# Kernel optimization log

Hardware: AMD Instinct MI355X
Metric: run time of the kernel (lower is better)

## Reference

```python
import jax, jax.numpy as jnp
import numpy as np

DIM = 2048
NH = 16
Q_LORA = 1536
KV_LORA = 512
NOPE = 128
ROPE = 64
VDIM = 128
QK = NOPE + ROPE  # 192
B, S = 2, 2048
EPS = 1.1920929e-07  # torch.finfo(float32).eps (nn.RMSNorm default)


def linear(x, w, b):
    return jnp.einsum('...i,oi->...o', x, w) + b


def rmsnorm(x, w):
    ms = jnp.mean(x * x, axis=-1, keepdims=True)
    return x * jax.lax.rsqrt(ms + EPS) * w


def rope(x, cos, sin):
    # x: [B,S,H,d] interleaved pairs; cos/sin: [S, d//2]
    x = x.reshape(*x.shape[:-1], -1, 2)
    x0, x1 = x[..., 0], x[..., 1]
    c = cos[None, :, None, :]
    s = sin[None, :, None, :]
    y0 = x0 * c - x1 * s
    y1 = x0 * s + x1 * c
    return jnp.stack([y0, y1], axis=-1).reshape(*x.shape[:-2], -1)


def setup_inputs() -> dict:
    key = jax.random.key(0)
    ks = jax.random.split(key, 12)
    sd = 0.02
    x = jax.random.normal(ks[0], (B, S, DIM), dtype=jnp.float32)
    freqs = jax.random.normal(ks[1], (S, ROPE // 2), dtype=jnp.float32)
    causal_mask = jnp.where(jnp.triu(jnp.ones((S, S), bool), k=1), -1e9, 0.0).astype(jnp.float32)
    inp = dict(x=x, freqs=freqs, causal_mask=causal_mask)
    inp['Wq_down_w'] = sd * jax.random.normal(ks[2], (Q_LORA, DIM), dtype=jnp.float32)
    inp['Wq_down_b'] = jnp.zeros((Q_LORA,), jnp.float32)
    inp['q_norm_w'] = jnp.ones((Q_LORA,), jnp.float32)
    inp['Wq_up_w'] = sd * jax.random.normal(ks[3], (NH * QK, Q_LORA), dtype=jnp.float32)
    inp['Wq_up_b'] = jnp.zeros((NH * QK,), jnp.float32)
    inp['Wkv_down_w'] = sd * jax.random.normal(ks[4], (KV_LORA + ROPE, DIM), dtype=jnp.float32)
    inp['Wkv_down_b'] = jnp.zeros((KV_LORA + ROPE,), jnp.float32)
    inp['kv_norm_w'] = jnp.ones((KV_LORA,), jnp.float32)
    inp['Wkv_up_w'] = sd * jax.random.normal(ks[5], (NH * (NOPE + VDIM), KV_LORA), dtype=jnp.float32)
    inp['Wkv_up_b'] = jnp.zeros((NH * (NOPE + VDIM),), jnp.float32)
    inp['Wo_w'] = sd * jax.random.normal(ks[6], (DIM, NH * VDIM), dtype=jnp.float32)
    inp['Wo_b'] = jnp.zeros((DIM,), jnp.float32)
    return inp


def reference(x, freqs, causal_mask, Wq_down_w, Wq_down_b, q_norm_w, Wq_up_w, Wq_up_b,
              Wkv_down_w, Wkv_down_b, kv_norm_w, Wkv_up_w, Wkv_up_b, Wo_w, Wo_b):
    cos, sin = jnp.cos(freqs), jnp.sin(freqs)
    scale = QK ** -0.5
    # Q path: low-rank down, RMSNorm, up
    q_lat = rmsnorm(linear(x, Wq_down_w, Wq_down_b), q_norm_w)
    Q = linear(q_lat, Wq_up_w, Wq_up_b).reshape(B, S, NH, QK)
    Q_nope, Q_rope = Q[..., :NOPE], Q[..., NOPE:]
    Q_rope = rope(Q_rope, cos, sin)
    Q = jnp.concatenate([Q_nope, Q_rope], axis=-1)  # [B,S,H,QK]
    # KV path: shared latent + decoupled rope key
    kv_kr = linear(x, Wkv_down_w, Wkv_down_b)
    kv_lat, K_rope = kv_kr[..., :KV_LORA], kv_kr[..., KV_LORA:]
    kv_lat = rmsnorm(kv_lat, kv_norm_w)
    K_rope = rope(K_rope[:, :, None, :], cos, sin)  # [B,S,1,ROPE]
    kv = linear(kv_lat, Wkv_up_w, Wkv_up_b).reshape(B, S, NH, NOPE + VDIM)
    K_nope, V = kv[..., :NOPE], kv[..., NOPE:]
    K = jnp.concatenate([K_nope, jnp.broadcast_to(K_rope, (B, S, NH, ROPE))], axis=-1)
    # attention
    scores = jnp.einsum('bqhd,bkhd->bhqk', Q, K) * scale + causal_mask[None, None]
    attn = jax.nn.softmax(scores, axis=-1)
    out = jnp.einsum('bhqk,bkhd->bqhd', attn, V).reshape(B, S, NH * VDIM)
    return linear(out, Wo_w, Wo_b)
```

## Files before the change

kernel.cpp:

```cpp
#include <hip/hip_runtime.h>
#include <hip/hip_bf16.h>

#define DIMD 2048
#define NHD 16
#define QLORA 1536
#define KVLORA 512
#define QKD 192
#define BBD 2
#define SSD 2048
#define BSD (BBD*SSD)
#define KVPAD 640
#define BHN (BBD*NHD)
#define EPSF 1.1920929e-07f
#define SCALEF 0.07216878364870322f

typedef __hip_bfloat16 bf16;
typedef __attribute__((ext_vector_type(8))) short short8;
typedef __attribute__((ext_vector_type(4))) float floatx4;

typedef __attribute__((address_space(1))) char as1_char;
typedef __attribute__((address_space(3))) char as3_char;
#define GLD16(g, l) __builtin_amdgcn_global_load_lds((as1_char*)(g), (as3_char*)(l), 16, 0, 0)

__device__ __forceinline__ float block_sum(float x) {
#pragma unroll
  for (int o = 32; o > 0; o >>= 1) x += __shfl_xor(x, o, 64);
  __shared__ float red[4];
  __syncthreads();
  if ((threadIdx.x & 63) == 0) red[threadIdx.x >> 6] = x;
  __syncthreads();
  return red[0] + red[1] + red[2] + red[3];
}

template<bool STORE_BF16>
__global__ __launch_bounds__(256)
void gemm_bt(const bf16* __restrict__ A, const bf16* __restrict__ Bm,
             const float* __restrict__ bias, void* __restrict__ Cp,
             int M, int N, int K, long sA, long sB, long sC, int ldc)
{
  int m0 = blockIdx.y * 128, n0 = blockIdx.x * 128;
  long z = blockIdx.z;
  A  += z * sA;
  Bm += z * sB;

  __shared__ __align__(16) bf16 Asm[128 * 32];
  __shared__ __align__(16) bf16 Bsm[128 * 32];

  const int tid  = threadIdx.x;
  const int lane = tid & 63;
  const int wv   = tid >> 6;
  const int wm   = (wv >> 1) << 6;
  const int wn   = (wv & 1) << 6;
  const int fr   = lane & 15;
  const int q8   = (lane >> 4) << 3;

  floatx4 acc[4][4];
#pragma unroll
  for (int i = 0; i < 4; ++i)
#pragma unroll
    for (int j = 0; j < 4; ++j)
      acc[i][j] = (floatx4){0.f, 0.f, 0.f, 0.f};

  for (int k0 = 0; k0 < K; k0 += 32) {
    __syncthreads();
#pragma unroll
    for (int it = 0; it < 2; ++it) {
      int seg = it * 256 + tid;
      int row = seg >> 2, cs = seg & 3;
      GLD16(A  + (long)(m0 + row) * K + k0 + cs * 8, &Asm[(it * 256 + wv * 64) * 8]);
      GLD16(Bm + (long)(n0 + row) * K + k0 + cs * 8, &Bsm[(it * 256 + wv * 64) * 8]);
    }
    __syncthreads();

    short8 fa[4], fb[4];
#pragma unroll
    for (int t = 0; t < 4; ++t) fa[t] = *(const short8*)&Asm[(wm + t * 16 + fr) * 32 + q8];
#pragma unroll
    for (int t = 0; t < 4; ++t) fb[t] = *(const short8*)&Bsm[(wn + t * 16 + fr) * 32 + q8];
#pragma unroll
    for (int i = 0; i < 4; ++i)
#pragma unroll
      for (int j = 0; j < 4; ++j)
        acc[i][j] = __builtin_amdgcn_mfma_f32_16x16x32_bf16(fa[i], fb[j], acc[i][j], 0, 0, 0);
  }

  long cb = z * sC;
  int rq = (lane >> 4) * 4;
#pragma unroll
  for (int i = 0; i < 4; ++i) {
#pragma unroll
    for (int j = 0; j < 4; ++j) {
      int col = n0 + wn + j * 16 + fr;
      float bv = bias ? bias[col] : 0.f;
#pragma unroll
      for (int r = 0; r < 4; ++r) {
        int rowg = m0 + wm + i * 16 + rq + r;
        float v = acc[i][j][r] + bv;
        if (STORE_BF16)
          ((bf16*)Cp)[cb + (long)rowg * ldc + col] = __float2bfloat16(v);
        else
          ((float*)Cp)[cb + (long)rowg * ldc + col] = v;
      }
    }
  }
}

__global__ __launch_bounds__(512, 2)
void flash_attn(const bf16* __restrict__ Qh, const bf16* __restrict__ Kh,
                const bf16* __restrict__ Vt, bf16* __restrict__ attnall)
{
  const int p = blockIdx.x;
  const int z = blockIdx.y;
  const int b = z >> 4, h = z & 15;

  const bf16* Qg = Qh + (long)z * SSD * QKD;
  const bf16* Kg = Kh + (long)z * SSD * QKD;
  const bf16* Vg = Vt + (long)z * 128 * SSD;

  __shared__ __align__(16) bf16 Ksm[6 * 4096];
  __shared__ __align__(16) bf16 Vsm[4 * 4096];
  bf16* Psm = Ksm;

  const int tid  = threadIdx.x;
  const int lane = tid & 63;
  const int wv   = tid >> 6;
  const int fr   = lane & 15;
  const int g4   = lane >> 4;
  const int q8   = g4 << 3;
  const int srow = tid >> 2;
  const int scs  = tid & 3;

#pragma unroll 1
  for (int t = 0; t < 2; ++t) {
    const int qt = t ? p : 15 - p;
    const int q0 = qt * 128;

    __syncthreads();
#pragma unroll
    for (int c = 0; c < 6; ++c)
      GLD16(Qg + (long)(q0 + srow) * QKD + c * 32 + scs * 8, &Ksm[c * 4096 + wv * 512]);
    __syncthreads();
    short8 qf[6];
#pragma unroll
    for (int c = 0; c < 6; ++c)
      qf[c] = *(const short8*)&Ksm[c * 4096 + (wv * 16 + fr) * 32 + q8];

    floatx4 oacc[8];
#pragma unroll
    for (int n = 0; n < 8; ++n) oacc[n] = (floatx4){0.f, 0.f, 0.f, 0.f};
    float mi[4], li[4];
#pragma unroll
    for (int r = 0; r < 4; ++r) { mi[r] = -1e30f; li[r] = 0.f; }

    for (int j = 0; j <= qt; ++j) {
      const int jb = j * 128;
      __syncthreads();
#pragma unroll
      for (int c = 0; c < 6; ++c)
        GLD16(Kg + (long)(jb + srow) * QKD + c * 32 + scs * 8, &Ksm[c * 4096 + wv * 512]);
#pragma unroll
      for (int c = 0; c < 4; ++c)
        GLD16(Vg + (long)srow * SSD + jb + c * 32 + scs * 8, &Vsm[c * 4096 + wv * 512]);
      __syncthreads();

      floatx4 sacc[8];
#pragma unroll
      for (int n = 0; n < 8; ++n) sacc[n] = (floatx4){0.f, 0.f, 0.f, 0.f};
#pragma unroll
      for (int c = 0; c < 6; ++c) {
#pragma unroll
        for (int n = 0; n < 8; ++n) {
          short8 fb = *(const short8*)&Ksm[c * 4096 + (n * 16 + fr) * 32 + q8];
          sacc[n] = __builtin_amdgcn_mfma_f32_16x16x32_bf16(qf[c], fb, sacc[n], 0, 0, 0);
        }
      }

      const bool diag = (j == qt);
#pragma unroll
      for (int r = 0; r < 4; ++r) {
        int rowg = q0 + wv * 16 + g4 * 4 + r;
        float mx = -1e30f;
#pragma unroll
        for (int n = 0; n < 8; ++n) {
          float v = sacc[n][r] * SCALEF;
          if (diag && (jb + n * 16 + fr) > rowg) v = -1e30f;
          sacc[n][r] = v;
          mx = fmaxf(mx, v);
        }
#pragma unroll
        for (int off = 1; off < 16; off <<= 1) mx = fmaxf(mx, __shfl_xor(mx, off, 64));
        float mnew = fmaxf(mi[r], mx);
        float alpha = __expf(mi[r] - mnew);
        mi[r] = mnew;
        float rs = 0.f;
#pragma unroll
        for (int n = 0; n < 8; ++n) {
          float pv = __expf(sacc[n][r] - mnew);
          sacc[n][r] = pv;
          rs += pv;
        }
#pragma unroll
        for (int off = 1; off < 16; off <<= 1) rs += __shfl_xor(rs, off, 64);
        li[r] = li[r] * alpha + rs;
#pragma unroll
        for (int n = 0; n < 8; ++n) oacc[n][r] *= alpha;
      }

      __syncthreads();
#pragma unroll
      for (int n = 0; n < 8; ++n) {
        int c2 = n >> 1;
        int col = (n & 1) * 16 + fr;
#pragma unroll
        for (int r = 0; r < 4; ++r) {
          int m = wv * 16 + g4 * 4 + r;
          Psm[c2 * 4096 + m * 32 + col] = __float2bfloat16(sacc[n][r]);
        }
      }

#pragma unroll
      for (int c2 = 0; c2 < 4; ++c2) {
        short8 pf = *(const short8*)&Psm[c2 * 4096 + (wv * 16 + fr) * 32 + q8];
#pragma unroll
        for (int dn = 0; dn < 8; ++dn) {
          short8 vf = *(const short8*)&Vsm[c2 * 4096 + (dn * 16 + fr) * 32 + q8];
          oacc[dn] = __builtin_amdgcn_mfma_f32_16x16x32_bf16(pf, vf, oacc[dn], 0, 0, 0);
        }
      }
    }

#pragma unroll
    for (int r = 0; r < 4; ++r) {
      float inv = 1.f / li[r];
      int m = q0 + wv * 16 + g4 * 4 + r;
      bf16* orow = attnall + ((long)(b * SSD + m) * NHD + h) * 128;
#pragma unroll
      for (int dn = 0; dn < 8; ++dn)
        orow[dn * 16 + fr] = __float2bfloat16(oacc[dn][r] * inv);
    }
  }
}

__device__ __forceinline__ void cvt4(const float* __restrict__ s, bf16* __restrict__ d,
                                     long se, long de) {
  float4 v = *(const float4*)(s + se);
  union { bf16 h[4]; uint2 u; } o;
  o.h[0] = __float2bfloat16(v.x); o.h[1] = __float2bfloat16(v.y);
  o.h[2] = __float2bfloat16(v.z); o.h[3] = __float2bfloat16(v.w);
  *(uint2*)(d + de) = o.u;
}

#define NX4   ((long)BSD * DIMD / 4)
#define NQD4  ((long)QLORA * DIMD / 4)
#define NQU4  ((long)3072 * QLORA / 4)
#define NKVD4 ((long)KVPAD * DIMD / 4)
#define NKVU4 ((long)4096 * KVLORA / 4)
#define NWO4  ((long)DIMD * 2048 / 4)

__global__ __launch_bounds__(256)
void cvt_all(const float* __restrict__ x, const float* __restrict__ wqd,
             const float* __restrict__ wqu, const float* __restrict__ wkvd,
             const float* __restrict__ wkvu, const float* __restrict__ wo,
             bf16* __restrict__ dx, bf16* __restrict__ dwqd, bf16* __restrict__ dwqu,
             bf16* __restrict__ dwkvd, bf16* __restrict__ dwkvu, bf16* __restrict__ dwo)
{
  long i = (long)blockIdx.x * 256 + threadIdx.x;
  if (i < NX4) { cvt4(x, dx, i * 4, i * 4); return; }
  i -= NX4;
  if (i < NQD4) { cvt4(wqd, dwqd, i * 4, i * 4); return; }
  i -= NQD4;
  if (i < NQU4) { cvt4(wqu, dwqu, i * 4, i * 4); return; }
  i -= NQU4;
  if (i < NKVD4) {
    long e = i * 4;
    long r = e >> 11;
    if (r < 576) cvt4(wkvd, dwkvd, e, e);
    else *(uint2*)(dwkvd + e) = (uint2){0u, 0u};
    return;
  }
  i -= NKVD4;
  if (i < NKVU4) { cvt4(wkvu, dwkvu, i * 4, i * 4); return; }
  i -= NKVU4;
  if (i < NWO4) { cvt4(wo, dwo, i * 4, i * 4); return; }
}

template<int L>
__global__ __launch_bounds__(256)
void rmsnorm_k(const bf16* __restrict__ in, const float* __restrict__ bias,
               const float* __restrict__ w, bf16* __restrict__ out, int ldin)
{
  constexpr int NIT = L / 256;
  long r = blockIdx.x;
  const bf16* row = in + r * ldin;
  int tid = threadIdx.x;
  float v[NIT];
  float ss = 0.f;
#pragma unroll
  for (int i = 0; i < NIT; ++i) {
    int c = tid + (i << 8);
    float x = __bfloat162float(row[c]) + (bias ? bias[c] : 0.f);
    v[i] = x;
    ss += x * x;
  }
  ss = block_sum(ss);
  float sc = rsqrtf(ss / (float)L + EPSF);
#pragma unroll
  for (int i = 0; i < NIT; ++i) {
    int c = tid + (i << 8);
    out[r * L + c] = __float2bfloat16(v[i] * sc * w[c]);
  }
}

__global__ void build_q(const bf16* __restrict__ Qf, const float* __restrict__ freqs,
                        bf16* __restrict__ Qh)
{
  int idx = blockIdx.x * 256 + threadIdx.x;
  if (idx >= BSD * NHD * 96) return;
  int j = idx % 96;
  int h = (idx / 96) % NHD;
  int srow = idx / (96 * NHD);
  int s = srow & (SSD - 1);
  int b = srow >> 11;
  const bf16* src = Qf + (long)srow * (NHD * QKD) + h * QKD + 2 * j;
  float x0 = __bfloat162float(src[0]), x1 = __bfloat162float(src[1]), y0, y1;
  if (j >= 64) {
    int i = j - 64;
    float f = freqs[s * 32 + i];
    float c = cosf(f), sn = sinf(f);
    y0 = x0 * c - x1 * sn;
    y1 = x0 * sn + x1 * c;
  } else { y0 = x0; y1 = x1; }
  bf16* dst = Qh + ((long)(b * NHD + h) * SSD + s) * QKD + 2 * j;
  dst[0] = __float2bfloat16(y0);
  dst[1] = __float2bfloat16(y1);
}

__global__ void build_k(const bf16* __restrict__ kvf, const bf16* __restrict__ kvkr,
                        const float* __restrict__ kvb, const float* __restrict__ freqs,
                        bf16* __restrict__ Kh)
{
  int idx = blockIdx.x * 256 + threadIdx.x;
  if (idx >= BSD * NHD * 96) return;
  int j = idx % 96;
  int h = (idx / 96) % NHD;
  int srow = idx / (96 * NHD);
  int s = srow & (SSD - 1);
  int b = srow >> 11;
  float y0, y1;
  if (j < 64) {
    const bf16* src = kvf + (long)srow * 4096 + h * 256 + 2 * j;
    y0 = __bfloat162float(src[0]); y1 = __bfloat162float(src[1]);
  } else {
    int i = j - 64;
    float x0 = __bfloat162float(kvkr[(long)srow * KVPAD + 512 + 2 * i]) + kvb[512 + 2 * i];
    float x1 = __bfloat162float(kvkr[(long)srow * KVPAD + 513 + 2 * i]) + kvb[513 + 2 * i];
    float f = freqs[s * 32 + i];
    float c = cosf(f), sn = sinf(f);
    y0 = x0 * c - x1 * sn;
    y1 = x0 * sn + x1 * c;
  }
  bf16* dst = Kh + ((long)(b * NHD + h) * SSD + s) * QKD + 2 * j;
  dst[0] = __float2bfloat16(y0);
  dst[1] = __float2bfloat16(y1);
}

__global__ __launch_bounds__(256)
void build_vt(const bf16* __restrict__ kvf, bf16* __restrict__ Vt)
{
  __shared__ float t[32][33];
  int s0 = blockIdx.x * 32, d0 = blockIdx.y * 32, z = blockIdx.z;
  int b = z / NHD, h = z % NHD;
  int tx = threadIdx.x, ty = threadIdx.y;
#pragma unroll
  for (int r = 0; r < 4; ++r) {
    int sl = ty + r * 8;
    t[sl][tx] = __bfloat162float(kvf[(long)(b * SSD + s0 + sl) * 4096 + h * 256 + 128 + d0 + tx]);
  }
  __syncthreads();
#pragma unroll
  for (int r = 0; r < 4; ++r) {
    int dl = ty + r * 8;
    Vt[((long)z * 128 + d0 + dl) * SSD + s0 + tx] = __float2bfloat16(t[tx][dl]);
  }
}

__global__ void diag_fill(float* out) { out[blockIdx.x * 256 + threadIdx.x] = 1000.0f; }

extern "C" void kernel_launch(void* const* d_in, const int* in_sizes, int n_in,
                              void* d_out, int out_size, void* d_ws, size_t ws_size,
                              hipStream_t stream)
{
  const float* x     = (const float*)d_in[0];
  const float* freqs = (const float*)d_in[1];
  const float* Wqd   = (const float*)d_in[3];
  const float* Wqdb  = (const float*)d_in[4];
  const float* qnw   = (const float*)d_in[5];
  const float* Wqu   = (const float*)d_in[6];
  const float* Wqub  = (const float*)d_in[7];
  const float* Wkvd  = (const float*)d_in[8];
  const float* Wkvdb = (const float*)d_in[9];
  const float* kvnw  = (const float*)d_in[10];
  const float* Wkvu  = (const float*)d_in[11];
  const float* Wkvub = (const float*)d_in[12];
  const float* Wo    = (const float*)d_in[13];
  const float* Wob   = (const float*)d_in[14];
  float* out = (float*)d_out;

  char* ws = (char*)d_ws;
  size_t off = 0;
  auto alloc = [&](size_t bytes) {
    void* p = ws + off;
    off += (bytes + 255) & ~(size_t)255;
    return p;
  };

  bf16* Wqd16  = (bf16*)alloc((size_t)QLORA * DIMD * 2);
  bf16* Wqu16  = (bf16*)alloc((size_t)3072 * QLORA * 2);
  bf16* Wkvd16 = (bf16*)alloc((size_t)KVPAD * DIMD * 2);
  bf16* Wkvu16 = (bf16*)alloc((size_t)4096 * KVLORA * 2);
  bf16* Wo16   = (bf16*)alloc((size_t)DIMD * 2048 * 2);
  bf16* x16    = (bf16*)alloc((size_t)BSD * DIMD * 2);
  bf16* Ra     = (bf16*)alloc((size_t)BSD * QLORA * 2);
  bf16* Rb     = (bf16*)alloc((size_t)BSD * QLORA * 2);
  bf16* Rc     = (bf16*)alloc((size_t)BSD * 4096 * 2);
  bf16* Qh16   = (bf16*)alloc((size_t)BHN * SSD * QKD * 2);
  bf16* Kh16   = (bf16*)alloc((size_t)BHN * SSD * QKD * 2);
  bf16* Vt16   = (bf16*)alloc((size_t)BHN * 128 * SSD * 2);

  bf16* qdown   = Ra;  bf16* kvkr    = Ra;
  bf16* qlat16  = Rb;  bf16* kvlat16 = Rb;
  bf16* Qf      = Rc;  bf16* kvf     = Rc;  bf16* attnall = Rc;

  if (off > ws_size) { diag_fill<<<8, 256, 0, stream>>>(out); return; }

  dim3 blk(256);
  auto cdiv = [](long a, long b) { return (int)((a + b - 1) / b); };

  long tot4 = NX4 + NQD4 + NQU4 + NKVD4 + NKVU4 + NWO4;
  cvt_all<<<cdiv(tot4, 256), blk, 0, stream>>>(x, Wqd, Wqu, Wkvd, Wkvu, Wo,
                                               x16, Wqd16, Wqu16, Wkvd16, Wkvu16, Wo16);

  gemm_bt<true><<<dim3(QLORA / 128, BSD / 128, 1), blk, 0, stream>>>(
      x16, Wqd16, Wqdb, qdown, BSD, QLORA, DIMD, 0, 0, 0, QLORA);
  rmsnorm_k<QLORA><<<BSD, blk, 0, stream>>>(qdown, nullptr, qnw, qlat16, QLORA);
  gemm_bt<true><<<dim3(3072 / 128, BSD / 128, 1), blk, 0, stream>>>(
      qlat16, Wqu16, Wqub, Qf, BSD, 3072, QLORA, 0, 0, 0, 3072);
  build_q<<<cdiv((long)BSD * NHD * 96, 256), blk, 0, stream>>>(Qf, freqs, Qh16);

  gemm_bt<true><<<dim3(KVPAD / 128, BSD / 128, 1), blk, 0, stream>>>(
      x16, Wkvd16, nullptr, kvkr, BSD, KVPAD, DIMD, 0, 0, 0, KVPAD);
  rmsnorm_k<KVLORA><<<BSD, blk, 0, stream>>>(kvkr, Wkvdb, kvnw, kvlat16, KVPAD);
  gemm_bt<true><<<dim3(4096 / 128, BSD / 128, 1), blk, 0, stream>>>(
      kvlat16, Wkvu16, Wkvub, kvf, BSD, 4096, KVLORA, 0, 0, 0, 4096);
  build_k<<<cdiv((long)BSD * NHD * 96, 256), blk, 0, stream>>>(kvf, kvkr, Wkvdb, freqs, Kh16);
  build_vt<<<dim3(SSD / 32, 128 / 32, BHN), dim3(32, 8), 0, stream>>>(kvf, Vt16);

  flash_attn<<<dim3(8, BHN), dim3(512), 0, stream>>>(Qh16, Kh16, Vt16, attnall);

  gemm_bt<false><<<dim3(2048 / 128, BSD / 128, 1), blk, 0, stream>>>(
      attnall, Wo16, Wob, out, BSD, DIMD, 2048, 0, 0, 0, DIMD);
}
```

Before: 570.8 us.

## Triple-buffer K/V tiles in flash attention with swizzled LDS and causal wave skipping

```diff
diff --git a/kernel.cpp b/kernel.cpp
--- a/kernel.cpp
+++ b/kernel.cpp
@@ -109,41 +109,84 @@
 void flash_attn(const bf16* __restrict__ Qh, const bf16* __restrict__ Kh,
                 const bf16* __restrict__ Vt, bf16* __restrict__ attnall)
 {
-  const int p = blockIdx.x;
-  const int z = blockIdx.y;
+  const int p = blockIdx.y;
+  const int z = blockIdx.x;
   const int b = z >> 4, h = z & 15;
 
   const bf16* Qg = Qh + (long)z * SSD * QKD;
   const bf16* Kg = Kh + (long)z * SSD * QKD;
   const bf16* Vg = Vt + (long)z * 128 * SSD;
 
-  __shared__ __align__(16) bf16 Ksm[6 * 4096];
-  __shared__ __align__(16) bf16 Vsm[4 * 4096];
-  bf16* Psm = Ksm;
+  __shared__ __align__(16) bf16 KB[3][6 * 2048];
+  __shared__ __align__(16) bf16 VB[3][2 * 4096];
+  __shared__ __align__(16) bf16 PB[2 * 4096];
 
   const int tid  = threadIdx.x;
   const int lane = tid & 63;
   const int wv   = tid >> 6;
   const int fr   = lane & 15;
   const int g4   = lane >> 4;
-  const int q8   = g4 << 3;
-  const int srow = tid >> 2;
-  const int scs  = tid & 3;
+
+  long kofs[3]; int kdst[3];
+#pragma unroll
+  for (int it = 0; it < 3; ++it) {
+    int gseg = it * 512 + tid;
+    int c = gseg >> 8, rs = gseg & 255;
+    int r = rs >> 2, s = (rs & 3) ^ ((r >> 1) & 3);
+    kofs[it] = (long)r * QKD + c * 32 + s * 8;
+    kdst[it] = c * 2048 + rs * 8;
+  }
+  long vofs[2]; int vdst[2];
+#pragma unroll
+  for (int it = 0; it < 2; ++it) {
+    int gseg = it * 512 + tid;
+    int c2 = gseg >> 9, ds = gseg & 511;
+    int d = ds >> 2, s = (ds & 3) ^ ((d >> 1) & 3);
+    vofs[it] = (long)d * SSD + c2 * 32 + s * 8;
+    vdst[it] = c2 * 4096 + ds * 8;
+  }
+  const int qrow = wv * 16 + fr;
+  const int prow_off = qrow * 32 + (((g4 ^ (qrow >> 1)) & 3) << 3);
+  int fsw[4];
+#pragma unroll
+  for (int n = 0; n < 4; ++n) {
+    int row = n * 16 + fr;
+    fsw[n] = row * 32 + (((g4 ^ (row >> 1)) & 3) << 3);
+  }
+  int vsw[8];
+#pragma unroll
+  for (int dn = 0; dn < 8; ++dn) {
+    int row = dn * 16 + fr;
+    vsw[dn] = row * 32 + (((g4 ^ (row >> 1)) & 3) << 3);
+  }
+  const int qr = tid >> 2;
+  const int qs = (tid & 3) ^ ((qr >> 1) & 3);
+
+  auto stageKV = [&](int jb2, bf16* kb2, bf16* vb2) {
+#pragma unroll
+    for (int it = 0; it < 3; ++it)
+      GLD16(Kg + (long)jb2 * QKD + kofs[it], kb2 + kdst[it]);
+#pragma unroll
+    for (int it = 0; it < 2; ++it)
+      GLD16(Vg + jb2 + vofs[it], vb2 + vdst[it]);
+  };
 
 #pragma unroll 1
   for (int t = 0; t < 2; ++t) {
     const int qt = t ? p : 15 - p;
-    const int q0 = qt * 128;
+    const int q0 = qt << 7;
+    const int jmax = 2 * qt + 1;
 
     __syncthreads();
 #pragma unroll
     for (int c = 0; c < 6; ++c)
-      GLD16(Qg + (long)(q0 + srow) * QKD + c * 32 + scs * 8, &Ksm[c * 4096 + wv * 512]);
+      GLD16(Qg + (long)(q0 + qr) * QKD + c * 32 + qs * 8, &KB[0][0] + c * 4096 + tid * 8);
     __syncthreads();
     short8 qf[6];
 #pragma unroll
     for (int c = 0; c < 6; ++c)
-      qf[c] = *(const short8*)&Ksm[c * 4096 + (wv * 16 + fr) * 32 + q8];
+      qf[c] = *(const short8*)(&KB[0][0] + c * 4096 + prow_off);
+    __syncthreads();
 
     floatx4 oacc[8];
 #pragma unroll
@@ -152,81 +195,101 @@
 #pragma unroll
     for (int r = 0; r < 4; ++r) { mi[r] = -1e30f; li[r] = 0.f; }
 
-    for (int j = 0; j <= qt; ++j) {
-      const int jb = j * 128;
-      __syncthreads();
-#pragma unroll
-      for (int c = 0; c < 6; ++c)
-        GLD16(Kg + (long)(jb + srow) * QKD + c * 32 + scs * 8, &Ksm[c * 4096 + wv * 512]);
-#pragma unroll
-      for (int c = 0; c < 4; ++c)
-        GLD16(Vg + (long)srow * SSD + jb + c * 32 + scs * 8, &Vsm[c * 4096 + wv * 512]);
-      __syncthreads();
-
-      floatx4 sacc[8];
-#pragma unroll
-      for (int n = 0; n < 8; ++n) sacc[n] = (floatx4){0.f, 0.f, 0.f, 0.f};
-#pragma unroll
-      for (int c = 0; c < 6; ++c) {
-#pragma unroll
-        for (int n = 0; n < 8; ++n) {
-          short8 fb = *(const short8*)&Ksm[c * 4096 + (n * 16 + fr) * 32 + q8];
-          sacc[n] = __builtin_amdgcn_mfma_f32_16x16x32_bf16(qf[c], fb, sacc[n], 0, 0, 0);
+    stageKV(0, &KB[0][0], &VB[0][0]);
+    if (jmax >= 1) stageKV(64, &KB[1][0], &VB[1][0]);
+
+#pragma unroll 1
+    for (int j = 0; j <= jmax; ++j) {
+      const int jb = j << 6;
+      if (j + 2 <= jmax) {
+        const int bi = (j + 2) % 3;
+        stageKV((j + 2) << 6, &KB[bi][0], &VB[bi][0]);
+        asm volatile("s_waitcnt vmcnt(10)" ::: "memory");
+      } else if (j + 1 <= jmax) {
+        asm volatile("s_waitcnt vmcnt(5)" ::: "memory");
+      } else {
+        asm volatile("s_waitcnt vmcnt(0)" ::: "memory");
+      }
+      __builtin_amdgcn_sched_barrier(0);
+      __builtin_amdgcn_s_barrier();
+      __builtin_amdgcn_sched_barrier(0);
+
+      const bf16* kb = &KB[j % 3][0];
+      const bf16* vb = &VB[j % 3][0];
+      const bool active = (jb <= q0 + wv * 16 + 15);
+      if (active) {
+        floatx4 sacc[4];
+#pragma unroll
+        for (int n = 0; n < 4; ++n) sacc[n] = (floatx4){0.f, 0.f, 0.f, 0.f};
+        __builtin_amdgcn_s_setprio(1);
+#pragma unroll
+        for (int c = 0; c < 6; ++c) {
+#pragma unroll
+          for (int n = 0; n < 4; ++n) {
+            short8 fb = *(const short8*)(kb + c * 2048 + fsw[n]);
+            sacc[n] = __builtin_amdgcn_mfma_f32_16x16x32_bf16(qf[c], fb, sacc[n], 0, 0, 0);
+          }
         }
+        __builtin_amdgcn_s_setprio(0);
+
+        const bool diag = (jb + 63 > q0 + wv * 16);
+#pragma unroll
+        for (int r = 0; r < 4; ++r) {
+          int rowg = q0 + wv * 16 + g4 * 4 + r;
+          float mx = -1e30f;
+#pragma unroll
+          for (int n = 0; n < 4; ++n) {
+            float v = sacc[n][r] * SCALEF;
+            if (diag && (jb + n * 16 + fr) > rowg) v = -1e30f;
+            sacc[n][r] = v;
+            mx = fmaxf(mx, v);
+          }
+#pragma unroll
+          for (int off = 1; off < 16; off <<= 1) mx = fmaxf(mx, __shfl_xor(mx, off, 64));
+          float mnew = fmaxf(mi[r], mx);
+          float alpha = __expf(mi[r] - mnew);
+          mi[r] = mnew;
+          float rs = 0.f;
+#pragma unroll
+          for (int n = 0; n < 4; ++n) {
+            float pv = __expf(sacc[n][r] - mnew);
+            sacc[n][r] = pv;
+            rs += pv;
+          }
+#pragma unroll
+          for (int off = 1; off < 16; off <<= 1) rs += __shfl_xor(rs, off, 64);
+          li[r] = li[r] * alpha + rs;
+#pragma unroll
+          for (int n = 0; n < 8; ++n) oacc[n][r] *= alpha;
+        }
+
+#pragma unroll
+        for (int n = 0; n < 4; ++n) {
+          int c2 = n >> 1;
+          int col = (n & 1) * 16 + fr;
+#pragma unroll
+          for (int r = 0; r < 4; ++r) {
+            int m = wv * 16 + g4 * 4 + r;
+            int cw = (((col >> 3) ^ ((m >> 1) & 3)) << 3) | (col & 7);
+            PB[c2 * 4096 + m * 32 + cw] = __float2bfloat16(sacc[n][r]);
+          }
+        }
+
+        __builtin_amdgcn_s_setprio(1);
+#pragma unroll
+        for (int c2 = 0; c2 < 2; ++c2) {
+          short8 pf = *(const short8*)&PB[c2 * 4096 + prow_off];
+#pragma unroll
+          for (int dn = 0; dn < 8; ++dn) {
+            short8 vf = *(const short8*)(vb + c2 * 4096 + vsw[dn]);
+            oacc[dn] = __builtin_amdgcn_mfma_f32_16x16x32_bf16(pf, vf, oacc[dn], 0, 0, 0);
+          }
+        }
+        __builtin_amdgcn_s_setprio(0);
       }
-
-      const bool diag = (j == qt);
-#pragma unroll
-      for (int r = 0; r < 4; ++r) {
-        int rowg = q0 + wv * 16 + g4 * 4 + r;
-        float mx = -1e30f;
-#pragma unroll
-        for (int n = 0; n < 8; ++n) {
-          float v = sacc[n][r] * SCALEF;
-          if (diag && (jb + n * 16 + fr) > rowg) v = -1e30f;
-          sacc[n][r] = v;
-          mx = fmaxf(mx, v);
-        }
-#pragma unroll
-        for (int off = 1; off < 16; off <<= 1) mx = fmaxf(mx, __shfl_xor(mx, off, 64));
-        float mnew = fmaxf(mi[r], mx);
-        float alpha = __expf(mi[r] - mnew);
-        mi[r] = mnew;
-        float rs = 0.f;
-#pragma unroll
-        for (int n = 0; n < 8; ++n) {
-          float pv = __expf(sacc[n][r] - mnew);
-          sacc[n][r] = pv;
-          rs += pv;
-        }
-#pragma unroll
-        for (int off = 1; off < 16; off <<= 1) rs += __shfl_xor(rs, off, 64);
-        li[r] = li[r] * alpha + rs;
-#pragma unroll
-        for (int n = 0; n < 8; ++n) oacc[n][r] *= alpha;
-      }
-
-      __syncthreads();
-#pragma unroll
-      for (int n = 0; n < 8; ++n) {
-        int c2 = n >> 1;
-        int col = (n & 1) * 16 + fr;
-#pragma unroll
-        for (int r = 0; r < 4; ++r) {
-          int m = wv * 16 + g4 * 4 + r;
-          Psm[c2 * 4096 + m * 32 + col] = __float2bfloat16(sacc[n][r]);
-        }
-      }
-
-#pragma unroll
-      for (int c2 = 0; c2 < 4; ++c2) {
-        short8 pf = *(const short8*)&Psm[c2 * 4096 + (wv * 16 + fr) * 32 + q8];
-#pragma unroll
-        for (int dn = 0; dn < 8; ++dn) {
-          short8 vf = *(const short8*)&Vsm[c2 * 4096 + (dn * 16 + fr) * 32 + q8];
-          oacc[dn] = __builtin_amdgcn_mfma_f32_16x16x32_bf16(pf, vf, oacc[dn], 0, 0, 0);
-        }
-      }
+      __builtin_amdgcn_sched_barrier(0);
+      __builtin_amdgcn_s_barrier();
+      __builtin_amdgcn_sched_barrier(0);
     }
 
 #pragma unroll
@@ -455,7 +518,7 @@
   build_k<<<cdiv((long)BSD * NHD * 96, 256), blk, 0, stream>>>(kvf, kvkr, Wkvdb, freqs, Kh16);
   build_vt<<<dim3(SSD / 32, 128 / 32, BHN), dim3(32, 8), 0, stream>>>(kvf, Vt16);
 
-  flash_attn<<<dim3(8, BHN), dim3(512), 0, stream>>>(Qh16, Kh16, Vt16, attnall);
+  flash_attn<<<dim3(BHN, 8), dim3(512), 0, stream>>>(Qh16, Kh16, Vt16, attnall);
 
   gemm_bt<false><<<dim3(2048 / 128, BSD / 128, 1), blk, 0, stream>>>(
       attnall, Wo16, Wob, out, BSD, DIMD, 2048, 0, 0, 0, DIMD);
```

Result: no change. 567.2 us (-0.6%).
